# Kernel optimization log

Hardware: AMD Instinct MI355X
Metric: run time of the kernel (lower is better)

The kernel has to match this reference:

```python
import jax, jax.numpy as jnp
import numpy as np

EMBED_DIM = 1024
NUM_HEADS = 16
HEAD_DIM = EMBED_DIM // NUM_HEADS


def setup_inputs() -> dict:
    key = jax.random.key(0)
    ks = jax.random.split(key, 5)
    B, N = 4, 2048
    s_in = 1.0 / np.sqrt(EMBED_DIM)
    return {
        "x": jax.random.normal(ks[0], (B, N, EMBED_DIM), dtype=jnp.float32),
        "qkv_w": jax.random.uniform(ks[1], (3 * EMBED_DIM, EMBED_DIM), jnp.float32, -s_in, s_in),
        "qkv_b": jax.random.uniform(ks[2], (3 * EMBED_DIM,), jnp.float32, -s_in, s_in),
        "o_w": jax.random.uniform(ks[3], (EMBED_DIM, EMBED_DIM), jnp.float32, -s_in, s_in),
        "o_b": jax.random.uniform(ks[4], (EMBED_DIM,), jnp.float32, -s_in, s_in),
    }


def reference(x, qkv_w, qkv_b, o_w, o_b):
    B, N, E = x.shape
    H, D = NUM_HEADS, HEAD_DIM
    # qkv: [B, N, 3E] -> [B, N, H, 3D] -> [B, H, N, 3D], then chunk last dim
    qkv = (jnp.einsum('bne,fe->bnf', x, qkv_w) + qkv_b)
    qkv = qkv.reshape(B, N, H, 3 * D).transpose(0, 2, 1, 3)
    q, k, v = jnp.split(qkv, 3, axis=-1)
    scale = 1.0 / np.sqrt(D)
    scores = jnp.einsum('bhqd,bhkd->bhqk', q, k) * scale
    attn = jax.nn.softmax(scores, axis=-1)  # dropout is identity in eval mode
    out = jnp.einsum('bhqk,bhkd->bhqd', attn, v)
    out = out.transpose(0, 2, 1, 3).reshape(B, N, E)
    return jnp.einsum('bne,fe->bnf', out, o_w) + o_b
```

## Files before the change

kernel.cpp:

```cpp
#include <hip/hip_runtime.h>

typedef unsigned short u16;
typedef float f32x4 __attribute__((ext_vector_type(4)));
typedef float f32x16 __attribute__((ext_vector_type(16)));
typedef short bf16x8 __attribute__((ext_vector_type(8)));
typedef int i32x2 __attribute__((ext_vector_type(2)));

__device__ __forceinline__ u16 f2bf(float f){
  union { float f; unsigned u; } x; x.f = f;
  unsigned r = (x.u + 0x7FFFu + ((x.u >> 16) & 1u)) >> 16;
  return (u16)r;
}

__device__ __forceinline__ unsigned cvtpk(float lo, float hi){
  unsigned r;
  asm("v_cvt_pk_bf16_f32 %0, %1, %2" : "=v"(r) : "v"(lo), "v"(hi));
  return r;
}

__device__ __forceinline__ void exp4q(float& a, float& b, float& c, float& d){
  asm("v_exp_f32 %0, %0\n\t"
      "v_exp_f32 %1, %1\n\t"
      "v_exp_f32 %2, %2\n\t"
      "v_exp_f32 %3, %3\n\t"
      "s_nop 1"
      : "+v"(a), "+v"(b), "+v"(c), "+v"(d));
}

__device__ __forceinline__ f32x4 mfma_bf16(bf16x8 a, bf16x8 b, f32x4 c){
  return __builtin_amdgcn_mfma_f32_16x16x32_bf16(a, b, c, 0, 0, 0);
}

__device__ __forceinline__ f32x16 mfma32(bf16x8 a, bf16x8 b, f32x16 c){
  return __builtin_amdgcn_mfma_f32_32x32x16_bf16(a, b, c, 0, 0, 0);
}

__device__ __forceinline__ void gload16(const u16* g, u16* l){
  __builtin_amdgcn_global_load_lds((__attribute__((address_space(1))) void*)g,
                                   (__attribute__((address_space(3))) void*)l, 16, 0, 0);
}

__global__ void cvt_bf16(const float* __restrict__ in, u16* __restrict__ out, int n4){
  int stride = gridDim.x * blockDim.x;
  for (int i = blockIdx.x*blockDim.x + threadIdx.x; i < n4; i += stride){
    float4 v = ((const float4*)in)[i];
    ushort4 o;
    o.x = f2bf(v.x); o.y = f2bf(v.y); o.z = f2bf(v.z); o.w = f2bf(v.w);
    ((ushort4*)out)[i] = o;
  }
}

template<int NCH, int NTHR>
__device__ __forceinline__ void stage32(const u16* src, int ld, u16* lds, int tid){
#pragma unroll
  for (int i = 0; i < NCH/NTHR; i++){
    int c = i*NTHR + tid;
    int row = c >> 2, slot = c & 3;
    int col = ((slot ^ (row & 3)) << 3);
    gload16(src + (size_t)row*ld + col, lds + ((size_t)(c & ~63) << 3));
  }
}

template<int NTHR>
__device__ __forceinline__ void stage64(const u16* src, int ld, u16* lds, int tid){
#pragma unroll
  for (int i = 0; i < 512/NTHR; i++){
    int c = i*NTHR + tid;
    int row = c >> 3, slot = c & 7;
    int col = ((slot ^ (row & 7)) << 3);
    gload16(src + (size_t)row*ld + col, lds + ((size_t)(c & ~63) << 3));
  }
}

template<int MODE, int WROWS>
__launch_bounds__(WROWS*128)
__global__ void gemm_bt(const u16* __restrict__ A, const u16* __restrict__ Bw,
                        const float* __restrict__ bias,
                        u16* __restrict__ Qp, u16* __restrict__ Kp, u16* __restrict__ Vt,
                        float* __restrict__ Co, int M, int Nf, int K)
{
  constexpr int BM = WROWS*64;
  constexpr int NTHR = WROWS*128;
  __shared__ u16 lsA[2][BM*32];
  __shared__ u16 lsB[2][128*32];
  int tid = threadIdx.x;
  int wave = tid >> 6, lane = tid & 63, grp = lane >> 4, l16 = lane & 15;
  int ntn = Nf >> 7;
  int bm = blockIdx.x / ntn, bn = blockIdx.x % ntn;
  const u16* Ab = A + (size_t)bm*BM*K;
  const u16* Bb = Bw + (size_t)bn*128*K;
  int wm = wave >> 1, wn = wave & 1;
  f32x4 acc[4][4] = {};

  stage32<BM*4, NTHR>(Ab, K, lsA[0], tid);
  stage32<512,  NTHR>(Bb, K, lsB[0], tid);
  int nk = K >> 5;
  for (int t = 0; t < nk; t++){
    __syncthreads();
    int cur = t & 1;
    if (t + 1 < nk){
      stage32<BM*4, NTHR>(Ab + ((t+1) << 5), K, lsA[cur^1], tid);
      stage32<512,  NTHR>(Bb + ((t+1) << 5), K, lsB[cur^1], tid);
    }
    const u16* la = lsA[cur];
    const u16* lb = lsB[cur];
    bf16x8 af[4], bfr[4];
#pragma unroll
    for (int mf = 0; mf < 4; mf++){
      int row = wm*64 + mf*16 + l16;
      af[mf] = *(const bf16x8*)(la + row*32 + ((grp ^ (row & 3)) << 3));
    }
#pragma unroll
    for (int nf = 0; nf < 4; nf++){
      int row = wn*64 + nf*16 + l16;
      bfr[nf] = *(const bf16x8*)(lb + row*32 + ((grp ^ (row & 3)) << 3));
    }
#pragma unroll
    for (int mf = 0; mf < 4; mf++)
#pragma unroll
      for (int nf = 0; nf < 4; nf++)
        acc[mf][nf] = mfma_bf16(af[mf], bfr[nf], acc[mf][nf]);
  }

  int mrow0 = bm*BM + wm*64;
  int f0 = bn*128 + wn*64;
#pragma unroll
  for (int nf = 0; nf < 4; nf++){
    int f = f0 + nf*16 + l16;
    float bv = bias[f];
    if constexpr (MODE == 0){
      int h = f / 192, c = f % 192;
#pragma unroll
      for (int mf = 0; mf < 4; mf++){
        int mbase = mrow0 + mf*16 + grp*4;
        int bb = mbase >> 11, n0 = mbase & 2047;
        size_t bh = (size_t)bb*16 + h;
        if (c >= 128){
          ushort4 w;
          w.x = f2bf(acc[mf][nf][0] + bv);
          w.y = f2bf(acc[mf][nf][1] + bv);
          w.z = f2bf(acc[mf][nf][2] + bv);
          w.w = f2bf(acc[mf][nf][3] + bv);
          *(ushort4*)(Vt + (bh*64 + (size_t)(c - 128))*2048 + n0) = w;
        } else {
          u16* dst = (c < 64) ? Qp : Kp;
          float sc = (c < 64) ? 0.18033688011f : 1.0f;
          int cc = c & 63;
#pragma unroll
          for (int r = 0; r < 4; r++)
            dst[(bh*2048 + n0 + r)*64 + cc] = f2bf((acc[mf][nf][r] + bv) * sc);
        }
      }
    } else {
#pragma unroll
      for (int mf = 0; mf < 4; mf++){
        int mbase = mrow0 + mf*16 + grp*4;
#pragma unroll
        for (int r = 0; r < 4; r++)
          Co[(size_t)(mbase + r)*Nf + f] = acc[mf][nf][r] + bv;
      }
    }
  }
}

__launch_bounds__(512, 4)
__global__ void attn_fwd(const u16* __restrict__ Qg, const u16* __restrict__ Kg,
                         const u16* __restrict__ Vtg, u16* __restrict__ Oa)
{
  __shared__ u16 kl[2][64*64];
  __shared__ u16 vl[2][64*64];
  int tid = threadIdx.x;
  int lane = tid & 63, wave = tid >> 6;
  int q32 = lane & 31, hi = lane >> 5;
  int bid = (blockIdx.x & 7) * 64 + (blockIdx.x >> 3);
  int bh = bid >> 3, qt = bid & 7;
  int b = bh >> 4, h = bh & 15;
  int q0 = qt*256 + wave*32;
  const u16* Qb = Qg + ((size_t)bh*2048 + q0)*64;
  const u16* Kb = Kg + (size_t)bh*2048*64;
  const u16* Vb = Vtg + (size_t)bh*64*2048;

  bf16x8 qf[4];
#pragma unroll
  for (int s = 0; s < 4; s++)
    qf[s] = *(const bf16x8*)(Qb + q32*64 + s*16 + hi*8);

  f32x16 lacc = {};
  f32x16 oacc[2] = {};

  stage64<512>(Kb, 64, kl[0], tid);
  stage64<512>(Vb, 2048, vl[0], tid);

  for (int kt = 0; kt < 32; kt++){
    __syncthreads();
    int cur = kt & 1;
    if (kt + 1 < 32){
      stage64<512>(Kb + (size_t)(kt+1)*64*64, 64, kl[cur^1], tid);
      stage64<512>(Vb + (kt+1)*64, 2048, vl[cur^1], tid);
    }
    const u16* lk = kl[cur];
    const u16* lv = vl[cur];

    f32x16 p0 = {}, p1 = {};
    __builtin_amdgcn_s_setprio(1);
#pragma unroll
    for (int s = 0; s < 4; s++){
      int r0 = q32;
      bf16x8 k0 = *(const bf16x8*)(lk + r0*64 + (((s*2+hi) ^ (r0 & 7)) << 3));
      p0 = mfma32(k0, qf[s], p0);
      int r1 = 32 + q32;
      bf16x8 k1 = *(const bf16x8*)(lk + r1*64 + (((s*2+hi) ^ (r1 & 7)) << 3));
      p1 = mfma32(k1, qf[s], p1);
    }
    __builtin_amdgcn_s_setprio(0);

#pragma unroll
    for (int r = 0; r < 16; r += 4){
      float a = p0[r], bq = p0[r+1], cq = p0[r+2], d = p0[r+3];
      exp4q(a, bq, cq, d);
      p0[r] = a; p0[r+1] = bq; p0[r+2] = cq; p0[r+3] = d;
    }
#pragma unroll
    for (int r = 0; r < 16; r += 4){
      float a = p1[r], bq = p1[r+1], cq = p1[r+2], d = p1[r+3];
      exp4q(a, bq, cq, d);
      p1[r] = a; p1[r+1] = bq; p1[r+2] = cq; p1[r+3] = d;
    }
#pragma unroll
    for (int r = 0; r < 16; r++) lacc[r] += p0[r];
#pragma unroll
    for (int r = 0; r < 16; r++) lacc[r] += p1[r];

#pragma unroll
    for (int ks = 0; ks < 4; ks++){
      const f32x16& pp = (ks < 2) ? p0 : p1;
      int base = (ks & 1) * 8;
      unsigned t0 = cvtpk(pp[base+0], pp[base+1]);
      unsigned t1 = cvtpk(pp[base+2], pp[base+3]);
      unsigned t2 = cvtpk(pp[base+4], pp[base+5]);
      unsigned t3 = cvtpk(pp[base+6], pp[base+7]);
      i32x2 r02 = __builtin_amdgcn_permlane32_swap((int)t0, (int)t2, false, false);
      i32x2 r13 = __builtin_amdgcn_permlane32_swap((int)t1, (int)t3, false, false);
      union { unsigned u[4]; bf16x8 v; } pu;
      pu.u[0] = (unsigned)r02.x;
      pu.u[1] = (unsigned)r13.x;
      pu.u[2] = (unsigned)r02.y;
      pu.u[3] = (unsigned)r13.y;

      __builtin_amdgcn_s_setprio(1);
      int rowd0 = q32;
      bf16x8 v0 = *(const bf16x8*)(lv + rowd0*64 + (((ks*2+hi) ^ (rowd0 & 7)) << 3));
      oacc[0] = mfma32(v0, pu.v, oacc[0]);
      int rowd1 = 32 + q32;
      bf16x8 v1 = *(const bf16x8*)(lv + rowd1*64 + (((ks*2+hi) ^ (rowd1 & 7)) << 3));
      oacc[1] = mfma32(v1, pu.v, oacc[1]);
      __builtin_amdgcn_s_setprio(0);
    }
  }

#pragma unroll
  for (int r = 0; r < 8; r++) lacc[r] += lacc[r+8];
#pragma unroll
  for (int r = 0; r < 4; r++) lacc[r] += lacc[r+4];
  float l = (lacc[0] + lacc[1]) + (lacc[2] + lacc[3]);
  l += __shfl_xor(l, 32, 64);
  float inv = 1.0f / l;

  size_t obase = ((size_t)b*2048 + q0 + q32)*1024 + h*64;
#pragma unroll
  for (int dblk = 0; dblk < 2; dblk++)
#pragma unroll
    for (int rb = 0; rb < 4; rb++){
      ushort4 w;
      w.x = f2bf(oacc[dblk][rb*4+0] * inv);
      w.y = f2bf(oacc[dblk][rb*4+1] * inv);
      w.z = f2bf(oacc[dblk][rb*4+2] * inv);
      w.w = f2bf(oacc[dblk][rb*4+3] * inv);
      *(ushort4*)(Oa + obase + dblk*32 + rb*8 + hi*4) = w;
    }
}

extern "C" void kernel_launch(void* const* d_in, const int* in_sizes, int n_in,
                              void* d_out, int out_size, void* d_ws, size_t ws_size,
                              hipStream_t stream)
{
  const float* x    = (const float*)d_in[0];
  const float* qkvw = (const float*)d_in[1];
  const float* qkvb = (const float*)d_in[2];
  const float* ow   = (const float*)d_in[3];
  const float* ob   = (const float*)d_in[4];
  float* out = (float*)d_out;

  u16* xb = (u16*)d_ws;
  u16* wq = xb + (size_t)8192*1024;
  u16* wo = wq + (size_t)3072*1024;
  u16* Qp = wo + (size_t)1024*1024;
  u16* Kp = Qp + (size_t)64*2048*64;
  u16* Vt = Kp + (size_t)64*2048*64;
  u16* Oa = Vt + (size_t)64*2048*64;

  cvt_bf16<<<1024, 256, 0, stream>>>(x, xb, (8192*1024)/4);
  cvt_bf16<<<512, 256, 0, stream>>>(qkvw, wq, (3072*1024)/4);
  cvt_bf16<<<256, 256, 0, stream>>>(ow, wo, (1024*1024)/4);

  gemm_bt<0,4><<<32*24, 512, 0, stream>>>(xb, wq, qkvb, Qp, Kp, Vt, nullptr, 8192, 3072, 1024);
  attn_fwd<<<512, 512, 0, stream>>>(Qp, Kp, Vt, Oa);
  gemm_bt<1,2><<<64*8, 256, 0, stream>>>(Oa, wo, ob, nullptr, nullptr, nullptr, out, 8192, 1024, 1024);
}
```

Measured before the change: 198.1 us.

## Give each attention wave 64 query rows to reuse K/V fragments

The attention kernel now runs 4 waves per block instead of 8, and each wave handles two 32-row query tiles. Every K and V fragment read from LDS then feeds two MFMAs, which halves LDS read traffic per MFMA and batches the exp/pack work ahead of the PV MFMAs. The QKV GEMM launch also moves to a different template variant with 256 threads and twice as many blocks. In exchange, register pressure roughly doubles (launch bounds 256,2) and fewer waves are resident to hide latency.

```diff
diff --git a/kernel.cpp b/kernel.cpp
--- a/kernel.cpp
+++ b/kernel.cpp
@@ -2,6 +2,7 @@
 
 typedef unsigned short u16;
 typedef float f32x4 __attribute__((ext_vector_type(4)));
+typedef float f32x8 __attribute__((ext_vector_type(8)));
 typedef float f32x16 __attribute__((ext_vector_type(16)));
 typedef short bf16x8 __attribute__((ext_vector_type(8)));
 typedef int i32x2 __attribute__((ext_vector_type(2)));
@@ -163,7 +164,31 @@
   }
 }
 
-__launch_bounds__(512, 4)
+__device__ __forceinline__ bf16x8 packP(const f32x16& pp, int base){
+  unsigned t0 = cvtpk(pp[base+0], pp[base+1]);
+  unsigned t1 = cvtpk(pp[base+2], pp[base+3]);
+  unsigned t2 = cvtpk(pp[base+4], pp[base+5]);
+  unsigned t3 = cvtpk(pp[base+6], pp[base+7]);
+  i32x2 r02 = __builtin_amdgcn_permlane32_swap((int)t0, (int)t2, false, false);
+  i32x2 r13 = __builtin_amdgcn_permlane32_swap((int)t1, (int)t3, false, false);
+  union { unsigned u[4]; bf16x8 v; } pu;
+  pu.u[0] = (unsigned)r02.x;
+  pu.u[1] = (unsigned)r13.x;
+  pu.u[2] = (unsigned)r02.y;
+  pu.u[3] = (unsigned)r13.y;
+  return pu.v;
+}
+
+__device__ __forceinline__ void expv16(f32x16& p){
+#pragma unroll
+  for (int r = 0; r < 16; r += 4){
+    float a = p[r], b = p[r+1], c = p[r+2], d = p[r+3];
+    exp4q(a, b, c, d);
+    p[r] = a; p[r+1] = b; p[r+2] = c; p[r+3] = d;
+  }
+}
+
+__launch_bounds__(256, 2)
 __global__ void attn_fwd(const u16* __restrict__ Qg, const u16* __restrict__ Kg,
                          const u16* __restrict__ Vtg, u16* __restrict__ Oa)
 {
@@ -175,108 +200,108 @@
   int bid = (blockIdx.x & 7) * 64 + (blockIdx.x >> 3);
   int bh = bid >> 3, qt = bid & 7;
   int b = bh >> 4, h = bh & 15;
-  int q0 = qt*256 + wave*32;
+  int q0 = qt*256 + wave*64;
   const u16* Qb = Qg + ((size_t)bh*2048 + q0)*64;
   const u16* Kb = Kg + (size_t)bh*2048*64;
   const u16* Vb = Vtg + (size_t)bh*64*2048;
 
-  bf16x8 qf[4];
-#pragma unroll
-  for (int s = 0; s < 4; s++)
-    qf[s] = *(const bf16x8*)(Qb + q32*64 + s*16 + hi*8);
-
-  f32x16 lacc = {};
-  f32x16 oacc[2] = {};
-
-  stage64<512>(Kb, 64, kl[0], tid);
-  stage64<512>(Vb, 2048, vl[0], tid);
+  bf16x8 qfA[4], qfB[4];
+#pragma unroll
+  for (int s = 0; s < 4; s++){
+    qfA[s] = *(const bf16x8*)(Qb + q32*64 + s*16 + hi*8);
+    qfB[s] = *(const bf16x8*)(Qb + (32+q32)*64 + s*16 + hi*8);
+  }
+
+  f32x8 laccA = {}, laccB = {};
+  f32x16 oaccA[2] = {}, oaccB[2] = {};
+
+  stage64<256>(Kb, 64, kl[0], tid);
+  stage64<256>(Vb, 2048, vl[0], tid);
 
   for (int kt = 0; kt < 32; kt++){
     __syncthreads();
     int cur = kt & 1;
     if (kt + 1 < 32){
-      stage64<512>(Kb + (size_t)(kt+1)*64*64, 64, kl[cur^1], tid);
-      stage64<512>(Vb + (kt+1)*64, 2048, vl[cur^1], tid);
+      stage64<256>(Kb + (size_t)(kt+1)*64*64, 64, kl[cur^1], tid);
+      stage64<256>(Vb + (kt+1)*64, 2048, vl[cur^1], tid);
     }
     const u16* lk = kl[cur];
     const u16* lv = vl[cur];
 
-    f32x16 p0 = {}, p1 = {};
+    f32x16 p0A = {}, p1A = {}, p0B = {}, p1B = {};
     __builtin_amdgcn_s_setprio(1);
 #pragma unroll
     for (int s = 0; s < 4; s++){
       int r0 = q32;
       bf16x8 k0 = *(const bf16x8*)(lk + r0*64 + (((s*2+hi) ^ (r0 & 7)) << 3));
-      p0 = mfma32(k0, qf[s], p0);
       int r1 = 32 + q32;
       bf16x8 k1 = *(const bf16x8*)(lk + r1*64 + (((s*2+hi) ^ (r1 & 7)) << 3));
-      p1 = mfma32(k1, qf[s], p1);
+      p0A = mfma32(k0, qfA[s], p0A);
+      p0B = mfma32(k0, qfB[s], p0B);
+      p1A = mfma32(k1, qfA[s], p1A);
+      p1B = mfma32(k1, qfB[s], p1B);
     }
     __builtin_amdgcn_s_setprio(0);
 
-#pragma unroll
-    for (int r = 0; r < 16; r += 4){
-      float a = p0[r], bq = p0[r+1], cq = p0[r+2], d = p0[r+3];
-      exp4q(a, bq, cq, d);
-      p0[r] = a; p0[r+1] = bq; p0[r+2] = cq; p0[r+3] = d;
-    }
-#pragma unroll
-    for (int r = 0; r < 16; r += 4){
-      float a = p1[r], bq = p1[r+1], cq = p1[r+2], d = p1[r+3];
-      exp4q(a, bq, cq, d);
-      p1[r] = a; p1[r+1] = bq; p1[r+2] = cq; p1[r+3] = d;
-    }
-#pragma unroll
-    for (int r = 0; r < 16; r++) lacc[r] += p0[r];
-#pragma unroll
-    for (int r = 0; r < 16; r++) lacc[r] += p1[r];
-
+    expv16(p0A); expv16(p1A); expv16(p0B); expv16(p1B);
+#pragma unroll
+    for (int r = 0; r < 16; r++) laccA[r & 7] += p0A[r];
+#pragma unroll
+    for (int r = 0; r < 16; r++) laccA[r & 7] += p1A[r];
+#pragma unroll
+    for (int r = 0; r < 16; r++) laccB[r & 7] += p0B[r];
+#pragma unroll
+    for (int r = 0; r < 16; r++) laccB[r & 7] += p1B[r];
+
+    bf16x8 puA[4], puB[4];
 #pragma unroll
     for (int ks = 0; ks < 4; ks++){
-      const f32x16& pp = (ks < 2) ? p0 : p1;
-      int base = (ks & 1) * 8;
-      unsigned t0 = cvtpk(pp[base+0], pp[base+1]);
-      unsigned t1 = cvtpk(pp[base+2], pp[base+3]);
-      unsigned t2 = cvtpk(pp[base+4], pp[base+5]);
-      unsigned t3 = cvtpk(pp[base+6], pp[base+7]);
-      i32x2 r02 = __builtin_amdgcn_permlane32_swap((int)t0, (int)t2, false, false);
-      i32x2 r13 = __builtin_amdgcn_permlane32_swap((int)t1, (int)t3, false, false);
-      union { unsigned u[4]; bf16x8 v; } pu;
-      pu.u[0] = (unsigned)r02.x;
-      pu.u[1] = (unsigned)r13.x;
-      pu.u[2] = (unsigned)r02.y;
-      pu.u[3] = (unsigned)r13.y;
-
-      __builtin_amdgcn_s_setprio(1);
+      puA[ks] = packP((ks < 2) ? p0A : p1A, (ks & 1) * 8);
+      puB[ks] = packP((ks < 2) ? p0B : p1B, (ks & 1) * 8);
+    }
+
+    __builtin_amdgcn_s_setprio(1);
+#pragma unroll
+    for (int ks = 0; ks < 4; ks++){
       int rowd0 = q32;
       bf16x8 v0 = *(const bf16x8*)(lv + rowd0*64 + (((ks*2+hi) ^ (rowd0 & 7)) << 3));
-      oacc[0] = mfma32(v0, pu.v, oacc[0]);
       int rowd1 = 32 + q32;
       bf16x8 v1 = *(const bf16x8*)(lv + rowd1*64 + (((ks*2+hi) ^ (rowd1 & 7)) << 3));
-      oacc[1] = mfma32(v1, pu.v, oacc[1]);
-      __builtin_amdgcn_s_setprio(0);
-    }
-  }
-
-#pragma unroll
-  for (int r = 0; r < 8; r++) lacc[r] += lacc[r+8];
-#pragma unroll
-  for (int r = 0; r < 4; r++) lacc[r] += lacc[r+4];
-  float l = (lacc[0] + lacc[1]) + (lacc[2] + lacc[3]);
-  l += __shfl_xor(l, 32, 64);
-  float inv = 1.0f / l;
-
-  size_t obase = ((size_t)b*2048 + q0 + q32)*1024 + h*64;
+      oaccA[0] = mfma32(v0, puA[ks], oaccA[0]);
+      oaccB[0] = mfma32(v0, puB[ks], oaccB[0]);
+      oaccA[1] = mfma32(v1, puA[ks], oaccA[1]);
+      oaccB[1] = mfma32(v1, puB[ks], oaccB[1]);
+    }
+    __builtin_amdgcn_s_setprio(0);
+  }
+
+#pragma unroll
+  for (int r = 0; r < 4; r++) laccA[r] += laccA[r+4];
+#pragma unroll
+  for (int r = 0; r < 4; r++) laccB[r] += laccB[r+4];
+  float lA = (laccA[0] + laccA[1]) + (laccA[2] + laccA[3]);
+  float lB = (laccB[0] + laccB[1]) + (laccB[2] + laccB[3]);
+  lA += __shfl_xor(lA, 32, 64);
+  lB += __shfl_xor(lB, 32, 64);
+  float invA = 1.0f / lA, invB = 1.0f / lB;
+
+  size_t obaseA = ((size_t)b*2048 + q0 + q32)*1024 + h*64;
+  size_t obaseB = obaseA + (size_t)32*1024;
 #pragma unroll
   for (int dblk = 0; dblk < 2; dblk++)
 #pragma unroll
     for (int rb = 0; rb < 4; rb++){
-      ushort4 w;
-      w.x = f2bf(oacc[dblk][rb*4+0] * inv);
-      w.y = f2bf(oacc[dblk][rb*4+1] * inv);
-      w.z = f2bf(oacc[dblk][rb*4+2] * inv);
-      w.w = f2bf(oacc[dblk][rb*4+3] * inv);
-      *(ushort4*)(Oa + obase + dblk*32 + rb*8 + hi*4) = w;
+      ushort4 wA, wB;
+      wA.x = f2bf(oaccA[dblk][rb*4+0] * invA);
+      wA.y = f2bf(oaccA[dblk][rb*4+1] * invA);
+      wA.z = f2bf(oaccA[dblk][rb*4+2] * invA);
+      wA.w = f2bf(oaccA[dblk][rb*4+3] * invA);
+      *(ushort4*)(Oa + obaseA + dblk*32 + rb*8 + hi*4) = wA;
+      wB.x = f2bf(oaccB[dblk][rb*4+0] * invB);
+      wB.y = f2bf(oaccB[dblk][rb*4+1] * invB);
+      wB.z = f2bf(oaccB[dblk][rb*4+2] * invB);
+      wB.w = f2bf(oaccB[dblk][rb*4+3] * invB);
+      *(ushort4*)(Oa + obaseB + dblk*32 + rb*8 + hi*4) = wB;
     }
 }
 
@@ -303,7 +328,7 @@
   cvt_bf16<<<512, 256, 0, stream>>>(qkvw, wq, (3072*1024)/4);
   cvt_bf16<<<256, 256, 0, stream>>>(ow, wo, (1024*1024)/4);
 
-  gemm_bt<0,4><<<32*24, 512, 0, stream>>>(xb, wq, qkvb, Qp, Kp, Vt, nullptr, 8192, 3072, 1024);
-  attn_fwd<<<512, 512, 0, stream>>>(Qp, Kp, Vt, Oa);
+  gemm_bt<0,2><<<64*24, 256, 0, stream>>>(xb, wq, qkvb, Qp, Kp, Vt, nullptr, 8192, 3072, 1024);
+  attn_fwd<<<512, 256, 0, stream>>>(Qp, Kp, Vt, Oa);
   gemm_bt<1,2><<<64*8, 256, 0, stream>>>(Oa, wo, ob, nullptr, nullptr, nullptr, out, 8192, 1024, 1024);
 }
```

Result: no change. 197.9 us (-0.1%).

## Rewrite QKV GEMM with 256x256 tiles and a 4-stage LDS pipeline

Applied to the files above, without the earlier changes.

Replaces the templated QKV projection GEMM with a dedicated kernel that uses 256x256 output tiles, 8 waves, a 4-deep LDS ring buffer with explicit vmcnt waits, and prefetch loads interleaved between MFMA groups. An XCD-aware block remap is also added. The goal is more data reuse per loaded byte and better hiding of global-load latency behind MFMA work. In exchange it uses much more LDS (128KB) and more accumulator registers, which lowers occupancy. It also launches only 384 blocks, which may leave the wave tail uneven. The output GEMM and the attention helpers are only refactored.

```diff
diff --git a/kernel.cpp b/kernel.cpp
--- a/kernel.cpp
+++ b/kernel.cpp
@@ -50,15 +50,17 @@
   }
 }
 
+__device__ __forceinline__ void stage_chunk(const u16* src, int ld, u16* lds, int c){
+  int row = c >> 2, slot = c & 3;
+  int col = ((slot ^ (row & 3)) << 3);
+  gload16(src + (size_t)row*ld + col, lds + ((size_t)(c & ~63) << 3));
+}
+
 template<int NCH, int NTHR>
 __device__ __forceinline__ void stage32(const u16* src, int ld, u16* lds, int tid){
 #pragma unroll
-  for (int i = 0; i < NCH/NTHR; i++){
-    int c = i*NTHR + tid;
-    int row = c >> 2, slot = c & 3;
-    int col = ((slot ^ (row & 3)) << 3);
-    gload16(src + (size_t)row*ld + col, lds + ((size_t)(c & ~63) << 3));
-  }
+  for (int i = 0; i < NCH/NTHR; i++)
+    stage_chunk(src, ld, lds, i*NTHR + tid);
 }
 
 template<int NTHR>
@@ -72,35 +74,31 @@
   }
 }
 
-template<int MODE, int WROWS>
-__launch_bounds__(WROWS*128)
-__global__ void gemm_bt(const u16* __restrict__ A, const u16* __restrict__ Bw,
-                        const float* __restrict__ bias,
-                        u16* __restrict__ Qp, u16* __restrict__ Kp, u16* __restrict__ Vt,
-                        float* __restrict__ Co, int M, int Nf, int K)
+__launch_bounds__(256)
+__global__ void gemm_bt1(const u16* __restrict__ A, const u16* __restrict__ Bw,
+                         const float* __restrict__ bias, float* __restrict__ Co,
+                         int M, int Nf, int K)
 {
-  constexpr int BM = WROWS*64;
-  constexpr int NTHR = WROWS*128;
-  __shared__ u16 lsA[2][BM*32];
+  __shared__ u16 lsA[2][128*32];
   __shared__ u16 lsB[2][128*32];
   int tid = threadIdx.x;
   int wave = tid >> 6, lane = tid & 63, grp = lane >> 4, l16 = lane & 15;
   int ntn = Nf >> 7;
   int bm = blockIdx.x / ntn, bn = blockIdx.x % ntn;
-  const u16* Ab = A + (size_t)bm*BM*K;
+  const u16* Ab = A + (size_t)bm*128*K;
   const u16* Bb = Bw + (size_t)bn*128*K;
   int wm = wave >> 1, wn = wave & 1;
   f32x4 acc[4][4] = {};
 
-  stage32<BM*4, NTHR>(Ab, K, lsA[0], tid);
-  stage32<512,  NTHR>(Bb, K, lsB[0], tid);
+  stage32<512,256>(Ab, K, lsA[0], tid);
+  stage32<512,256>(Bb, K, lsB[0], tid);
   int nk = K >> 5;
   for (int t = 0; t < nk; t++){
     __syncthreads();
     int cur = t & 1;
     if (t + 1 < nk){
-      stage32<BM*4, NTHR>(Ab + ((t+1) << 5), K, lsA[cur^1], tid);
-      stage32<512,  NTHR>(Bb + ((t+1) << 5), K, lsB[cur^1], tid);
+      stage32<512,256>(Ab + ((t+1) << 5), K, lsA[cur^1], tid);
+      stage32<512,256>(Bb + ((t+1) << 5), K, lsB[cur^1], tid);
     }
     const u16* la = lsA[cur];
     const u16* lb = lsB[cur];
@@ -122,44 +120,149 @@
         acc[mf][nf] = mfma_bf16(af[mf], bfr[nf], acc[mf][nf]);
   }
 
-  int mrow0 = bm*BM + wm*64;
+  int mrow0 = bm*128 + wm*64;
   int f0 = bn*128 + wn*64;
 #pragma unroll
   for (int nf = 0; nf < 4; nf++){
     int f = f0 + nf*16 + l16;
     float bv = bias[f];
-    if constexpr (MODE == 0){
-      int h = f / 192, c = f % 192;
-#pragma unroll
-      for (int mf = 0; mf < 4; mf++){
-        int mbase = mrow0 + mf*16 + grp*4;
-        int bb = mbase >> 11, n0 = mbase & 2047;
-        size_t bh = (size_t)bb*16 + h;
-        if (c >= 128){
-          ushort4 w;
-          w.x = f2bf(acc[mf][nf][0] + bv);
-          w.y = f2bf(acc[mf][nf][1] + bv);
-          w.z = f2bf(acc[mf][nf][2] + bv);
-          w.w = f2bf(acc[mf][nf][3] + bv);
-          *(ushort4*)(Vt + (bh*64 + (size_t)(c - 128))*2048 + n0) = w;
-        } else {
-          u16* dst = (c < 64) ? Qp : Kp;
-          float sc = (c < 64) ? 0.18033688011f : 1.0f;
-          int cc = c & 63;
-#pragma unroll
-          for (int r = 0; r < 4; r++)
-            dst[(bh*2048 + n0 + r)*64 + cc] = f2bf((acc[mf][nf][r] + bv) * sc);
+#pragma unroll
+    for (int mf = 0; mf < 4; mf++){
+      int mbase = mrow0 + mf*16 + grp*4;
+#pragma unroll
+      for (int r = 0; r < 4; r++)
+        Co[(size_t)(mbase + r)*Nf + f] = acc[mf][nf][r] + bv;
+    }
+  }
+}
+
+__launch_bounds__(512, 2)
+__global__ void gemm_qkv(const u16* __restrict__ A, const u16* __restrict__ Bw,
+                         const float* __restrict__ bias,
+                         u16* __restrict__ Qp, u16* __restrict__ Kp,
+                         u16* __restrict__ Vt, int M, int Nf, int K)
+{
+  __shared__ u16 lsA[4][256*32];
+  __shared__ u16 lsB[4][256*32];
+  int tid = threadIdx.x;
+  int wave = tid >> 6, lane = tid & 63, grp = lane >> 4, l16 = lane & 15;
+  int ntn = Nf >> 8;
+  int bid = (blockIdx.x & 7) * 48 + (blockIdx.x >> 3);
+  int bm = bid / ntn, bn = bid % ntn;
+  const u16* Ab = A + (size_t)bm*256*K;
+  const u16* Bb = Bw + (size_t)bn*256*K;
+  int wr = wave >> 2, wc = wave & 3;
+  f32x4 acc[8][4] = {};
+
+#pragma unroll
+  for (int t = 0; t < 3; t++){
+    stage_chunk(Ab + (t << 5), K, lsA[t], tid);
+    stage_chunk(Ab + (t << 5), K, lsA[t], 512 + tid);
+    stage_chunk(Bb + (t << 5), K, lsB[t], tid);
+    stage_chunk(Bb + (t << 5), K, lsB[t], 512 + tid);
+  }
+  asm volatile("s_waitcnt vmcnt(8)" ::: "memory");
+  __builtin_amdgcn_s_barrier();
+  __builtin_amdgcn_sched_barrier(0);
+
+  int nk = K >> 5;
+  for (int t = 0; t < nk; t++){
+    const u16* la = lsA[t & 3];
+    const u16* lb = lsB[t & 3];
+    const u16* As = Ab + ((t + 3) << 5);
+    const u16* Bs = Bb + ((t + 3) << 5);
+    u16* dA = lsA[(t + 3) & 3];
+    u16* dB = lsB[(t + 3) & 3];
+    bool pf = (t + 3) < nk;
+    bf16x8 bfr[4];
+#pragma unroll
+    for (int p = 0; p < 4; p++){
+      int row0 = wr*128 + (2*p)*16 + l16;
+      bf16x8 af0 = *(const bf16x8*)(la + row0*32 + ((grp ^ (row0 & 3)) << 3));
+      int row1 = row0 + 16;
+      bf16x8 af1 = *(const bf16x8*)(la + row1*32 + ((grp ^ (row1 & 3)) << 3));
+      if (p == 0){
+#pragma unroll
+        for (int nf = 0; nf < 4; nf++){
+          int row = wc*64 + nf*16 + l16;
+          bfr[nf] = *(const bf16x8*)(lb + row*32 + ((grp ^ (row & 3)) << 3));
         }
       }
-    } else {
-#pragma unroll
-      for (int mf = 0; mf < 4; mf++){
-        int mbase = mrow0 + mf*16 + grp*4;
+      if (pf){
+        if (p < 2) stage_chunk(As, K, dA, p*512 + tid);
+        else       stage_chunk(Bs, K, dB, (p-2)*512 + tid);
+      }
+      __builtin_amdgcn_s_barrier();
+      __builtin_amdgcn_sched_barrier(0);
+      __builtin_amdgcn_s_setprio(1);
+#pragma unroll
+      for (int nf = 0; nf < 4; nf++){
+        acc[2*p][nf]   = mfma_bf16(af0, bfr[nf], acc[2*p][nf]);
+        acc[2*p+1][nf] = mfma_bf16(af1, bfr[nf], acc[2*p+1][nf]);
+      }
+      __builtin_amdgcn_s_setprio(0);
+      if (p == 3){
+        if (t < nk-3)       asm volatile("s_waitcnt vmcnt(8)" ::: "memory");
+        else if (t == nk-3) asm volatile("s_waitcnt vmcnt(4)" ::: "memory");
+        else if (t == nk-2) asm volatile("s_waitcnt vmcnt(0)" ::: "memory");
+      }
+      __builtin_amdgcn_s_barrier();
+      __builtin_amdgcn_sched_barrier(0);
+    }
+  }
+
+  int mrow0 = bm*256 + wr*128;
+  int f0 = bn*256 + wc*64;
+#pragma unroll
+  for (int nf = 0; nf < 4; nf++){
+    int f = f0 + nf*16 + l16;
+    float bv = bias[f];
+    int h = f / 192, c = f % 192;
+#pragma unroll
+    for (int mf = 0; mf < 8; mf++){
+      int mbase = mrow0 + mf*16 + grp*4;
+      int bb = mbase >> 11, n0 = mbase & 2047;
+      size_t bh = (size_t)bb*16 + h;
+      if (c >= 128){
+        ushort4 w;
+        w.x = f2bf(acc[mf][nf][0] + bv);
+        w.y = f2bf(acc[mf][nf][1] + bv);
+        w.z = f2bf(acc[mf][nf][2] + bv);
+        w.w = f2bf(acc[mf][nf][3] + bv);
+        *(ushort4*)(Vt + (bh*64 + (size_t)(c - 128))*2048 + n0) = w;
+      } else {
+        u16* dst = (c < 64) ? Qp : Kp;
+        float sc = (c < 64) ? 0.18033688011f : 1.0f;
+        int cc = c & 63;
 #pragma unroll
         for (int r = 0; r < 4; r++)
-          Co[(size_t)(mbase + r)*Nf + f] = acc[mf][nf][r] + bv;
-      }
-    }
+          dst[(bh*2048 + n0 + r)*64 + cc] = f2bf((acc[mf][nf][r] + bv) * sc);
+      }
+    }
+  }
+}
+
+__device__ __forceinline__ bf16x8 packP(const f32x16& pp, int base){
+  unsigned t0 = cvtpk(pp[base+0], pp[base+1]);
+  unsigned t1 = cvtpk(pp[base+2], pp[base+3]);
+  unsigned t2 = cvtpk(pp[base+4], pp[base+5]);
+  unsigned t3 = cvtpk(pp[base+6], pp[base+7]);
+  i32x2 r02 = __builtin_amdgcn_permlane32_swap((int)t0, (int)t2, false, false);
+  i32x2 r13 = __builtin_amdgcn_permlane32_swap((int)t1, (int)t3, false, false);
+  union { unsigned u[4]; bf16x8 v; } pu;
+  pu.u[0] = (unsigned)r02.x;
+  pu.u[1] = (unsigned)r13.x;
+  pu.u[2] = (unsigned)r02.y;
+  pu.u[3] = (unsigned)r13.y;
+  return pu.v;
+}
+
+__device__ __forceinline__ void expv16(f32x16& p){
+#pragma unroll
+  for (int r = 0; r < 16; r += 4){
+    float a = p[r], b = p[r+1], c = p[r+2], d = p[r+3];
+    exp4q(a, b, c, d);
+    p[r] = a; p[r+1] = b; p[r+2] = c; p[r+3] = d;
   }
 }
 
@@ -214,18 +317,7 @@
     }
     __builtin_amdgcn_s_setprio(0);
 
-#pragma unroll
-    for (int r = 0; r < 16; r += 4){
-      float a = p0[r], bq = p0[r+1], cq = p0[r+2], d = p0[r+3];
-      exp4q(a, bq, cq, d);
-      p0[r] = a; p0[r+1] = bq; p0[r+2] = cq; p0[r+3] = d;
-    }
-#pragma unroll
-    for (int r = 0; r < 16; r += 4){
-      float a = p1[r], bq = p1[r+1], cq = p1[r+2], d = p1[r+3];
-      exp4q(a, bq, cq, d);
-      p1[r] = a; p1[r+1] = bq; p1[r+2] = cq; p1[r+3] = d;
-    }
+    expv16(p0); expv16(p1);
 #pragma unroll
     for (int r = 0; r < 16; r++) lacc[r] += p0[r];
 #pragma unroll
@@ -233,27 +325,14 @@
 
 #pragma unroll
     for (int ks = 0; ks < 4; ks++){
-      const f32x16& pp = (ks < 2) ? p0 : p1;
-      int base = (ks & 1) * 8;
-      unsigned t0 = cvtpk(pp[base+0], pp[base+1]);
-      unsigned t1 = cvtpk(pp[base+2], pp[base+3]);
-      unsigned t2 = cvtpk(pp[base+4], pp[base+5]);
-      unsigned t3 = cvtpk(pp[base+6], pp[base+7]);
-      i32x2 r02 = __builtin_amdgcn_permlane32_swap((int)t0, (int)t2, false, false);
-      i32x2 r13 = __builtin_amdgcn_permlane32_swap((int)t1, (int)t3, false, false);
-      union { unsigned u[4]; bf16x8 v; } pu;
-      pu.u[0] = (unsigned)r02.x;
-      pu.u[1] = (unsigned)r13.x;
-      pu.u[2] = (unsigned)r02.y;
-      pu.u[3] = (unsigned)r13.y;
-
+      bf16x8 pb = packP((ks < 2) ? p0 : p1, (ks & 1) * 8);
       __builtin_amdgcn_s_setprio(1);
       int rowd0 = q32;
       bf16x8 v0 = *(const bf16x8*)(lv + rowd0*64 + (((ks*2+hi) ^ (rowd0 & 7)) << 3));
-      oacc[0] = mfma32(v0, pu.v, oacc[0]);
+      oacc[0] = mfma32(v0, pb, oacc[0]);
       int rowd1 = 32 + q32;
       bf16x8 v1 = *(const bf16x8*)(lv + rowd1*64 + (((ks*2+hi) ^ (rowd1 & 7)) << 3));
-      oacc[1] = mfma32(v1, pu.v, oacc[1]);
+      oacc[1] = mfma32(v1, pb, oacc[1]);
       __builtin_amdgcn_s_setprio(0);
     }
   }
@@ -303,7 +382,7 @@
   cvt_bf16<<<512, 256, 0, stream>>>(qkvw, wq, (3072*1024)/4);
   cvt_bf16<<<256, 256, 0, stream>>>(ow, wo, (1024*1024)/4);
 
-  gemm_bt<0,4><<<32*24, 512, 0, stream>>>(xb, wq, qkvb, Qp, Kp, Vt, nullptr, 8192, 3072, 1024);
+  gemm_qkv<<<32*12, 512, 0, stream>>>(xb, wq, qkvb, Qp, Kp, Vt, 8192, 3072, 1024);
   attn_fwd<<<512, 512, 0, stream>>>(Qp, Kp, Vt, Oa);
-  gemm_bt<1,2><<<64*8, 256, 0, stream>>>(Oa, wo, ob, nullptr, nullptr, nullptr, out, 8192, 1024, 1024);
-}
+  gemm_bt1<<<64*8, 256, 0, stream>>>(Oa, wo, ob, out, 8192, 1024, 1024);
+}
```

Measured after the change: 218.8 us. +10.4%, slower.

## Deepen attention K/V prefetch to a 4-slot ring and retile QKV GEMM

Applied to the files above, without the earlier changes.

The attention kernel moves from a double-buffered K/V LDS stage to a 4-slot ring that keeps three tiles in flight. Each iteration now uses an explicit vmcnt wait plus a raw s_barrier instead of __syncthreads, to hide global-load latency better. This doubles LDS use per block to 64KB, which can cut how many blocks fit on a CU despite the launch bounds. Separately, the QKV projection GEMM switches to a 256-thread, smaller-tile configuration with twice as many blocks. The pack and exp code is pulled into helper functions without changing what it computes.

```diff
diff --git a/kernel.cpp b/kernel.cpp
--- a/kernel.cpp
+++ b/kernel.cpp
@@ -163,12 +163,36 @@
   }
 }
 
+__device__ __forceinline__ bf16x8 packP(const f32x16& pp, int base){
+  unsigned t0 = cvtpk(pp[base+0], pp[base+1]);
+  unsigned t1 = cvtpk(pp[base+2], pp[base+3]);
+  unsigned t2 = cvtpk(pp[base+4], pp[base+5]);
+  unsigned t3 = cvtpk(pp[base+6], pp[base+7]);
+  i32x2 r02 = __builtin_amdgcn_permlane32_swap((int)t0, (int)t2, false, false);
+  i32x2 r13 = __builtin_amdgcn_permlane32_swap((int)t1, (int)t3, false, false);
+  union { unsigned u[4]; bf16x8 v; } pu;
+  pu.u[0] = (unsigned)r02.x;
+  pu.u[1] = (unsigned)r13.x;
+  pu.u[2] = (unsigned)r02.y;
+  pu.u[3] = (unsigned)r13.y;
+  return pu.v;
+}
+
+__device__ __forceinline__ void expv16(f32x16& p){
+#pragma unroll
+  for (int r = 0; r < 16; r += 4){
+    float a = p[r], b = p[r+1], c = p[r+2], d = p[r+3];
+    exp4q(a, b, c, d);
+    p[r] = a; p[r+1] = b; p[r+2] = c; p[r+3] = d;
+  }
+}
+
 __launch_bounds__(512, 4)
 __global__ void attn_fwd(const u16* __restrict__ Qg, const u16* __restrict__ Kg,
                          const u16* __restrict__ Vtg, u16* __restrict__ Oa)
 {
-  __shared__ u16 kl[2][64*64];
-  __shared__ u16 vl[2][64*64];
+  __shared__ u16 kl[4][64*64];
+  __shared__ u16 vl[4][64*64];
   int tid = threadIdx.x;
   int lane = tid & 63, wave = tid >> 6;
   int q32 = lane & 31, hi = lane >> 5;
@@ -188,18 +212,24 @@
   f32x16 lacc = {};
   f32x16 oacc[2] = {};
 
-  stage64<512>(Kb, 64, kl[0], tid);
-  stage64<512>(Vb, 2048, vl[0], tid);
+#pragma unroll
+  for (int t = 0; t < 3; t++){
+    stage64<512>(Kb + (size_t)t*64*64, 64, kl[t], tid);
+    stage64<512>(Vb + t*64, 2048, vl[t], tid);
+  }
 
   for (int kt = 0; kt < 32; kt++){
-    __syncthreads();
-    int cur = kt & 1;
-    if (kt + 1 < 32){
-      stage64<512>(Kb + (size_t)(kt+1)*64*64, 64, kl[cur^1], tid);
-      stage64<512>(Vb + (kt+1)*64, 2048, vl[cur^1], tid);
-    }
-    const u16* lk = kl[cur];
-    const u16* lv = vl[cur];
+    if (kt < 30)       asm volatile("s_waitcnt vmcnt(4)" ::: "memory");
+    else if (kt == 30) asm volatile("s_waitcnt vmcnt(2)" ::: "memory");
+    else               asm volatile("s_waitcnt vmcnt(0)" ::: "memory");
+    __builtin_amdgcn_s_barrier();
+    __builtin_amdgcn_sched_barrier(0);
+    if (kt + 3 < 32){
+      stage64<512>(Kb + (size_t)(kt+3)*64*64, 64, kl[(kt+3)&3], tid);
+      stage64<512>(Vb + (kt+3)*64, 2048, vl[(kt+3)&3], tid);
+    }
+    const u16* lk = kl[kt & 3];
+    const u16* lv = vl[kt & 3];
 
     f32x16 p0 = {}, p1 = {};
     __builtin_amdgcn_s_setprio(1);
@@ -214,18 +244,7 @@
     }
     __builtin_amdgcn_s_setprio(0);
 
-#pragma unroll
-    for (int r = 0; r < 16; r += 4){
-      float a = p0[r], bq = p0[r+1], cq = p0[r+2], d = p0[r+3];
-      exp4q(a, bq, cq, d);
-      p0[r] = a; p0[r+1] = bq; p0[r+2] = cq; p0[r+3] = d;
-    }
-#pragma unroll
-    for (int r = 0; r < 16; r += 4){
-      float a = p1[r], bq = p1[r+1], cq = p1[r+2], d = p1[r+3];
-      exp4q(a, bq, cq, d);
-      p1[r] = a; p1[r+1] = bq; p1[r+2] = cq; p1[r+3] = d;
-    }
+    expv16(p0); expv16(p1);
 #pragma unroll
     for (int r = 0; r < 16; r++) lacc[r] += p0[r];
 #pragma unroll
@@ -233,27 +252,14 @@
 
 #pragma unroll
     for (int ks = 0; ks < 4; ks++){
-      const f32x16& pp = (ks < 2) ? p0 : p1;
-      int base = (ks & 1) * 8;
-      unsigned t0 = cvtpk(pp[base+0], pp[base+1]);
-      unsigned t1 = cvtpk(pp[base+2], pp[base+3]);
-      unsigned t2 = cvtpk(pp[base+4], pp[base+5]);
-      unsigned t3 = cvtpk(pp[base+6], pp[base+7]);
-      i32x2 r02 = __builtin_amdgcn_permlane32_swap((int)t0, (int)t2, false, false);
-      i32x2 r13 = __builtin_amdgcn_permlane32_swap((int)t1, (int)t3, false, false);
-      union { unsigned u[4]; bf16x8 v; } pu;
-      pu.u[0] = (unsigned)r02.x;
-      pu.u[1] = (unsigned)r13.x;
-      pu.u[2] = (unsigned)r02.y;
-      pu.u[3] = (unsigned)r13.y;
-
+      bf16x8 pb = packP((ks < 2) ? p0 : p1, (ks & 1) * 8);
       __builtin_amdgcn_s_setprio(1);
       int rowd0 = q32;
       bf16x8 v0 = *(const bf16x8*)(lv + rowd0*64 + (((ks*2+hi) ^ (rowd0 & 7)) << 3));
-      oacc[0] = mfma32(v0, pu.v, oacc[0]);
+      oacc[0] = mfma32(v0, pb, oacc[0]);
       int rowd1 = 32 + q32;
       bf16x8 v1 = *(const bf16x8*)(lv + rowd1*64 + (((ks*2+hi) ^ (rowd1 & 7)) << 3));
-      oacc[1] = mfma32(v1, pu.v, oacc[1]);
+      oacc[1] = mfma32(v1, pb, oacc[1]);
       __builtin_amdgcn_s_setprio(0);
     }
   }
@@ -303,7 +309,7 @@
   cvt_bf16<<<512, 256, 0, stream>>>(qkvw, wq, (3072*1024)/4);
   cvt_bf16<<<256, 256, 0, stream>>>(ow, wo, (1024*1024)/4);
 
-  gemm_bt<0,4><<<32*24, 512, 0, stream>>>(xb, wq, qkvb, Qp, Kp, Vt, nullptr, 8192, 3072, 1024);
+  gemm_bt<0,2><<<64*24, 256, 0, stream>>>(xb, wq, qkvb, Qp, Kp, Vt, nullptr, 8192, 3072, 1024);
   attn_fwd<<<512, 512, 0, stream>>>(Qp, Kp, Vt, Oa);
   gemm_bt<1,2><<<64*8, 256, 0, stream>>>(Oa, wo, ob, nullptr, nullptr, nullptr, out, 8192, 1024, 1024);
 }
```

Result: no change. 196.2 us (-1.0%).
